# Kernel optimization log

Hardware: AMD Instinct MI355X
Metric: run time of the kernel (lower is better)

Reference implementation:

```python
import jax, jax.numpy as jnp
import numpy as np

B, F, V, DW, H, K, T = 32, 2048, 12000, 300, 512, 3, 32
START_ID, END_ID = 1, 2
NEG = -1e9


def lstm(x, h, c, Wx, Wh, b):
    # BasicLSTMCell with forget_bias=1.0
    z = x @ Wx + h @ Wh + b  # [N, 4H]
    i, f, g, o = jnp.split(z, 4, axis=-1)
    c2 = jax.nn.sigmoid(f + 1.0) * c + jax.nn.sigmoid(i) * jnp.tanh(g)
    h2 = jax.nn.sigmoid(o) * jnp.tanh(c2)
    return h2, c2


def beam_decode(E, Wx, Wh, b, Wl, bl, img):
    Bn = img.shape[0]
    img_t = jnp.repeat(img, K, axis=0)  # tile_batch: [B*K, F]
    h = jnp.zeros((Bn * K, H), img.dtype)
    c = jnp.zeros_like(h)
    beam_lp = jnp.tile(jnp.array([0.0] + [NEG] * (K - 1), img.dtype), (Bn, 1))  # [B,K]
    prev = jnp.full((Bn, K), START_ID, jnp.int32)
    finished = jnp.zeros((Bn, K), bool)
    lengths = jnp.zeros((Bn, K), jnp.int32)
    ids = jnp.zeros((Bn, K, T), jnp.int32)
    end_row = jnp.where(jnp.arange(V) == END_ID, 0.0, NEG)  # finished beams only emit END

    def step(carry, t):
        h, c, beam_lp, prev, finished, lengths, ids = carry
        x = jnp.concatenate([E[prev.reshape(-1)], img_t], axis=-1)  # [B*K, DW+F]
        h2, c2 = lstm(x, h, c, Wx, Wh, b)
        lp = jax.nn.log_softmax(h2 @ Wl + bl).reshape(Bn, K, V)
        lp = jnp.where(finished[:, :, None], end_row, lp)
        total = (beam_lp[:, :, None] + lp).reshape(Bn, K * V)
        scores, idx = jax.lax.top_k(total, K)  # [B,K]
        parent = idx // V
        word = (idx % V).astype(jnp.int32)
        g2 = lambda a: jnp.take_along_axis(a, parent, axis=1)
        g3 = lambda a: jnp.take_along_axis(a, parent[:, :, None], axis=1)
        h2 = g3(h2.reshape(Bn, K, H)).reshape(Bn * K, H)
        c2 = g3(c2.reshape(Bn, K, H)).reshape(Bn * K, H)
        ids = g3(ids).at[:, :, t].set(word)  # reorder hypotheses, append word
        fin_p = g2(finished)
        len_p = g2(lengths)
        lengths = jnp.where(fin_p, len_p, len_p + 1)
        finished = fin_p | (word == END_ID)
        return (h2, c2, scores, word, finished, lengths, ids), None

    carry, _ = jax.lax.scan(step, (h, c, beam_lp, prev, finished, lengths, ids), jnp.arange(T))
    return carry[6], carry[5]  # ids [B,K,T], lengths [B,K]


def teacher_rnn(E, Wx, Wh, b, img_t, seq_inputs, lengths):
    # dynamic_rnn semantics: zero outputs and frozen state past sequence_length
    N, L = seq_inputs.shape
    emb = E[seq_inputs]  # [N, L, DW]
    h0 = jnp.zeros((N, H), E.dtype)
    c0 = jnp.zeros_like(h0)

    def step(carry, xs):
        h, c = carry
        x_t, t = xs
        xin = jnp.concatenate([x_t, img_t], axis=-1)
        h2, c2 = lstm(xin, h, c, Wx, Wh, b)
        active = (t < lengths)[:, None]
        h = jnp.where(active, h2, h)
        c = jnp.where(active, c2, c)
        return (h, c), jnp.where(active, h2, 0.0)

    _, outs = jax.lax.scan(step, (h0, c0), (emb.transpose(1, 0, 2), jnp.arange(L)))
    return outs.transpose(1, 0, 2)  # [N, L, H]


def setup_inputs() -> dict:
    key = jax.random.key(0)
    ks = jax.random.split(key, 6)
    return {
        "mean_image_features": jax.random.normal(ks[0], (B, F), jnp.float32),
        "embeddings": jax.random.normal(ks[1], (V, DW), jnp.float32) * 0.1,
        "Wx": jax.random.normal(ks[2], (DW + F, 4 * H), jnp.float32) / np.sqrt(DW + F),
        "Wh": jax.random.normal(ks[3], (H, 4 * H), jnp.float32) / np.sqrt(H),
        "b_lstm": jnp.zeros((4 * H,), jnp.float32),
        "W_logits": jax.random.normal(ks[4], (H, V), jnp.float32) / np.sqrt(H),
        "b_logits": jnp.zeros((V,), jnp.float32),
    }


def reference(mean_image_features, embeddings, Wx, Wh, b_lstm, W_logits, b_logits):
    Bn = mean_image_features.shape[0]
    ids, lengths = beam_decode(embeddings, Wx, Wh, b_lstm, W_logits, b_logits, mean_image_features)
    seq_inputs = jnp.concatenate(
        [jnp.full((Bn, K, 1), START_ID, jnp.int32), ids], axis=2
    ).reshape(Bn * K, T + 1)
    img_t = jnp.repeat(mean_image_features, K, axis=0)
    acts = teacher_rnn(embeddings, Wx, Wh, b_lstm, img_t, seq_inputs, lengths.reshape(-1))
    logits = (acts @ W_logits + b_logits).reshape(Bn, K, T + 1, V)
    return logits, jnp.argmax(logits, axis=-1).astype(jnp.int32)
```

## Files before the change

kernel.cpp:

```cpp
#include <hip/hip_runtime.h>
#include <hip/hip_bf16.h>
#include <math.h>

#define NB   32
#define FDIM 2048
#define VV   12000
#define DWW  300
#define HH   512
#define KW   3
#define TDEC 32
#define SEQ  33
#define NK   96
#define G4   2048
#define START_ID 1
#define END_ID   2
#define NROWS 3168
#define NLB   188
#define INTMX 0x7fffffff
#define FLOORF (-3.0e38f)

typedef float f4v __attribute__((ext_vector_type(4)));
__device__ __forceinline__ void nt_store4(float* p, float4 v){
  f4v t; t.x=v.x; t.y=v.y; t.z=v.z; t.w=v.w;
  __builtin_nontemporal_store(t, (f4v*)p);
}

__device__ __forceinline__ float sigf(float x){ return 1.0f/(1.0f+expf(-x)); }

__device__ __forceinline__ unsigned short f2b(float x){
  __hip_bfloat16 b = __float2bfloat16(x);
  return *reinterpret_cast<unsigned short*>(&b);
}

__device__ __forceinline__ void ins3(float v, int i, float tv[3], int ti[3]){
  if (v > tv[0] || (v == tv[0] && i < ti[0])){
    tv[2]=tv[1]; ti[2]=ti[1]; tv[1]=tv[0]; ti[1]=ti[0]; tv[0]=v; ti[0]=i;
  } else if (v > tv[1] || (v == tv[1] && i < ti[1])){
    tv[2]=tv[1]; ti[2]=ti[1]; tv[1]=v; ti[1]=i;
  } else if (v > tv[2] || (v == tv[2] && i < ti[2])){
    tv[2]=v; ti[2]=i;
  }
}

__device__ __forceinline__ void flag_arrive(int* cnt){
  __hip_atomic_fetch_add(cnt, 1, __ATOMIC_RELEASE, __HIP_MEMORY_SCOPE_AGENT);
}
__device__ __forceinline__ void flag_wait(int* cnt, int target){
  while (__hip_atomic_load(cnt, __ATOMIC_ACQUIRE, __HIP_MEMORY_SCOPE_AGENT) < target)
    __builtin_amdgcn_s_sleep(1);
}

struct SArgs {
  const float *E, *Wx, *Wh, *Wl, *blog;
  float *P, *c2, *h2s, *zp, *partA, *beam_lp, *rowamax;
  int *prev, *finished, *lengths, *parst;
  int *cnt0, *cnt1;
  void *Lst;
};

__global__ __launch_bounds__(128) void k_pimg(const float* __restrict__ img,
                                              const float* __restrict__ Wx,
                                              float* __restrict__ parts)
{
  int colb = blockIdx.x, fb = blockIdx.y, tid = threadIdx.x;
  int col = colb*128 + tid;
  int f0 = fb*128;
  __shared__ float s_img[32][128];
  for (int r=0;r<32;r++) s_img[r][tid] = img[r*FDIM + f0 + tid];
  __syncthreads();
  float acc[32];
  #pragma unroll
  for (int r=0;r<32;r++) acc[r]=0.f;
  for (int f2=0; f2<128; ++f2){
    float w = Wx[(size_t)(DWW + f0 + f2)*G4 + col];
    #pragma unroll
    for (int r=0;r<32;r++) acc[r] += w * s_img[r][f2];
  }
  #pragma unroll
  for (int r=0;r<32;r++) parts[(size_t)fb*(32*G4) + r*G4 + col] = acc[r];
}

__global__ __launch_bounds__(512) void k_prep(const float* __restrict__ parts,
    const float* __restrict__ bls, const float* __restrict__ blog,
    float* __restrict__ P, float* __restrict__ beam_lp, int* __restrict__ prev,
    int* __restrict__ finished, int* __restrict__ lengths, int* __restrict__ cnts,
    float* __restrict__ bamax)
{
  int bid = blockIdx.x, tid = threadIdx.x;
  int gid = bid*512 + tid;
  float s = bls[gid & (G4-1)];
  for (int fb=0; fb<16; ++fb) s += parts[(size_t)fb*(32*G4) + gid];
  P[gid] = s;
  if (bid==0 && tid<NK){
    beam_lp[tid] = (tid%KW==0)?0.f:-1e9f;
    prev[tid]=START_ID; finished[tid]=0; lengths[tid]=0;
  }
  if (bid==1 && tid<2*TDEC) cnts[tid]=0;
  if (bid==2){
    __shared__ float s_rf[8]; __shared__ int s_ri[8];
    float bv=FLOORF; int bi=INTMX;
    for (int i=tid;i<VV;i+=512){
      float v=blog[i];
      if (v>bv || (v==bv && i<bi)){ bv=v; bi=i; }
    }
    #pragma unroll
    for (int d=1;d<64;d<<=1){
      float ov=__shfl_xor(bv,d); int oi=__shfl_xor(bi,d);
      if (ov>bv || (ov==bv && oi<bi)){ bv=ov; bi=oi; }
    }
    if ((tid&63)==0){ s_rf[tid>>6]=bv; s_ri[tid>>6]=bi; }
    __syncthreads();
    if (tid==0){
      for (int w=1;w<8;w++)
        if (s_rf[w]>bv || (s_rf[w]==bv && s_ri[w]<bi)){ bv=s_rf[w]; bi=s_ri[w]; }
      bamax[0] = (float)bi;
    }
  }
}

__global__ __launch_bounds__(512) void k_step1(SArgs a, int t)
{
  int bid = blockIdx.x, tid = threadIdx.x;
  __shared__ float smem[96*17 + 16*64];
  __shared__ int sprev[NK], spar[NK];
  if (t>0 && tid<NK){ sprev[tid]=a.prev[tid]; spar[tid]=a.parst[(t-1)*NK+tid]; }
  __syncthreads();

  {
    int colblk = bid & 31, p = bid >> 5;
    int col0 = colblk*64;
    int ks = p*104, ke = ks+104; if (ke>812) ke=812;
    float* sA = smem;
    float* sB = smem + 96*17;
    int tx = tid&15, ty = tid>>4;
    float4 acc[3];
    #pragma unroll
    for (int r=0;r<3;r++) acc[r]=make_float4(0.f,0.f,0.f,0.f);
    for (int k0=ks;k0<ke;k0+=16){
      int bk = ke-k0; if (bk>16) bk=16;
      for (int i=tid;i<96*16;i+=512){
        int n=i>>4, kk=i&15;
        float v=0.f;
        if (kk<bk){
          int kg=k0+kk;
          if (kg<DWW){
            int w = (t==0)?START_ID:sprev[n];
            v = a.E[(size_t)w*DWW+kg];
          } else if (t>0){
            v = a.h2s[((size_t)(t-1)*NK + spar[n])*HH + (kg-DWW)];
          }
        }
        sA[n*17+kk]=v;
      }
      for (int i=tid;i<16*64;i+=512){
        int kk=i>>6, cc=i&63;
        float v=0.f;
        if (kk<bk){
          int kg=k0+kk;
          v = (kg<DWW) ? a.Wx[(size_t)kg*G4+col0+cc] : a.Wh[(size_t)(kg-DWW)*G4+col0+cc];
        }
        sB[i]=v;
      }
      __syncthreads();
      #pragma unroll
      for (int kk=0;kk<16;++kk){
        float4 b4 = *(const float4*)&sB[kk*64+tx*4];
        #pragma unroll
        for (int rr=0;rr<3;rr++){
          float av = sA[(ty+rr*32)*17+kk];
          acc[rr].x += av*b4.x; acc[rr].y += av*b4.y;
          acc[rr].z += av*b4.z; acc[rr].w += av*b4.w;
        }
      }
      __syncthreads();
    }
    float* zpp = a.zp + (size_t)p*NK*G4;
    #pragma unroll
    for (int rr=0;rr<3;rr++)
      *(float4*)&zpp[(size_t)(ty+rr*32)*G4 + col0 + tx*4] = acc[rr];
  }
  __syncthreads();
  if (tid==0) flag_arrive(&a.cnt0[t]);
  if (bid >= NK) return;

  if (tid==0) flag_wait(&a.cnt0[t], 256);
  __syncthreads();
  {
    int n = bid, m = tid, bb = n/KW;
    const float* Pr = a.P + (size_t)bb*G4;
    float zi=Pr[m], zf=Pr[HH+m], zg=Pr[2*HH+m], zo=Pr[3*HH+m];
    for (int p=0;p<8;p++){
      const float* zz = a.zp + (size_t)p*NK*G4 + (size_t)n*G4;
      zi+=zz[m]; zf+=zz[HH+m]; zg+=zz[2*HH+m]; zo+=zz[3*HH+m];
    }
    float cold = (t==0) ? 0.f : a.c2[(size_t)((t-1)&1)*NK*HH + (size_t)spar[n]*HH + m];
    float c2v = sigf(zf+1.0f)*cold + sigf(zi)*tanhf(zg);
    float h2v = sigf(zo)*tanhf(c2v);
    a.c2[(size_t)(t&1)*NK*HH + (size_t)n*HH + m] = c2v;
    a.h2s[((size_t)t*NK+n)*HH + m] = h2v;
  }
}

template<int BF>
__global__ __launch_bounds__(512) void k_step2(SArgs a, int t)
{
  int bid = blockIdx.x, tid = threadIdx.x;
  __shared__ float smem[96*36 + 32*64];
  __shared__ float s_lse[KW], s_tv3[KW*3];
  __shared__ int   s_ti3[KW*3];

  {
    int col0 = bid*64;
    float* sA = smem;
    float* sB = smem + 96*36;
    int tx=tid&15, ty=tid>>4;
    float4 acc[3];
    #pragma unroll
    for (int r=0;r<3;r++) acc[r]=make_float4(0.f,0.f,0.f,0.f);
    for (int k0=0;k0<HH;k0+=32){
      for (int i=tid;i<768;i+=512){
        int row=i>>3, kq=(i&7)*4;
        *(float4*)&sA[row*36+kq] = *(const float4*)&a.h2s[((size_t)t*NK+row)*HH + k0+kq];
      }
      {
        int kk=tid>>4, c4=(tid&15)*4;
        int col=col0+c4;
        float4 v = make_float4(0.f,0.f,0.f,0.f);
        if (col < VV) v = *(const float4*)&a.Wl[(size_t)(k0+kk)*VV+col];
        *(float4*)&sB[kk*64+c4]=v;
      }
      __syncthreads();
      #pragma unroll
      for (int kk=0;kk<32;++kk){
        float4 b4 = *(const float4*)&sB[kk*64+tx*4];
        #pragma unroll
        for (int rr=0;rr<3;rr++){
          float av = sA[(ty+rr*32)*36+kk];
          acc[rr].x += av*b4.x; acc[rr].y += av*b4.y;
          acc[rr].z += av*b4.z; acc[rr].w += av*b4.w;
        }
      }
      __syncthreads();
    }
    int colg = col0 + tx*4;
    bool cval = colg < VV;
    float4 bias = make_float4(0.f,0.f,0.f,0.f);
    if (cval) bias = *(const float4*)&a.blog[colg];
    #pragma unroll
    for (int rr=0;rr<3;rr++){
      int row = ty + rr*32;
      float v0,v1,v2,v3;
      if (cval){
        v0=acc[rr].x+bias.x; v1=acc[rr].y+bias.y;
        v2=acc[rr].z+bias.z; v3=acc[rr].w+bias.w;
        size_t off = (size_t)(t*NK+row)*VV + colg;
        if (BF){
          ushort4 u;
          u.x=f2b(v0); u.y=f2b(v1); u.z=f2b(v2); u.w=f2b(v3);
          *(ushort4*)((unsigned short*)a.Lst + off) = u;
        } else {
          *(float4*)((float*)a.Lst + off) = make_float4(v0,v1,v2,v3);
        }
      } else { v0=v1=v2=v3=-INFINITY; }
      float m = fmaxf(fmaxf(v0,v1),fmaxf(v2,v3));
      #pragma unroll
      for (int d=1;d<16;d<<=1) m = fmaxf(m,__shfl_xor(m,d));
      float tv[3]={-INFINITY,-INFINITY,-INFINITY};
      int   ti[3]={INTMX,INTMX,INTMX};
      float s=0.f;
      if (cval){
        ins3(v0,colg,tv,ti); ins3(v1,colg+1,tv,ti);
        ins3(v2,colg+2,tv,ti); ins3(v3,colg+3,tv,ti);
        s = expf(v0-m)+expf(v1-m)+expf(v2-m)+expf(v3-m);
      }
      #pragma unroll
      for (int d=1;d<16;d<<=1){
        s += __shfl_xor(s,d);
        float p0=__shfl_xor(tv[0],d),p1=__shfl_xor(tv[1],d),p2=__shfl_xor(tv[2],d);
        int q0=__shfl_xor(ti[0],d),q1=__shfl_xor(ti[1],d),q2=__shfl_xor(ti[2],d);
        ins3(p0,q0,tv,ti); ins3(p1,q1,tv,ti); ins3(p2,q2,tv,ti);
      }
      if (tx==0){
        float* rp = a.partA + ((size_t)row*NLB + bid)*8;
        *(float4*)rp = make_float4(m,s,tv[0],tv[1]);
        *((float4*)rp+1) = make_float4(tv[2],__int_as_float(ti[0]),__int_as_float(ti[1]),__int_as_float(ti[2]));
      }
    }
  }
  __syncthreads();
  if (tid==0) flag_arrive(&a.cnt1[t]);
  if (bid >= NB) return;

  if (tid==0) flag_wait(&a.cnt1[t], NLB);
  __syncthreads();
  {
    int b = bid;
    int wv = tid>>6, lane = tid&63;
    if (wv < KW){
      int n = b*KW+wv;
      float M=FLOORF, S=0.f;
      float tv[3]={FLOORF,FLOORF,FLOORF}; int ti[3]={INTMX,INTMX,INTMX};
      for (int i=lane;i<NLB;i+=64){
        const float* rp = a.partA + ((size_t)n*NLB+i)*8;
        float4 r0=*(const float4*)rp, r1=*((const float4*)rp+1);
        float nm = fmaxf(M,r0.x);
        S = S*expf(M-nm) + r0.y*expf(r0.x-nm);
        M = nm;
        ins3(r0.z,__float_as_int(r1.y),tv,ti);
        ins3(r0.w,__float_as_int(r1.z),tv,ti);
        ins3(r1.x,__float_as_int(r1.w),tv,ti);
      }
      #pragma unroll
      for (int d=1;d<64;d<<=1){
        float Mo=__shfl_xor(M,d), So=__shfl_xor(S,d);
        float nm=fmaxf(M,Mo);
        S = S*expf(M-nm)+So*expf(Mo-nm);
        M=nm;
        float p0=__shfl_xor(tv[0],d),p1=__shfl_xor(tv[1],d),p2=__shfl_xor(tv[2],d);
        int q0=__shfl_xor(ti[0],d),q1=__shfl_xor(ti[1],d),q2=__shfl_xor(ti[2],d);
        ins3(p0,q0,tv,ti); ins3(p1,q1,tv,ti); ins3(p2,q2,tv,ti);
      }
      if (lane==0){
        s_lse[wv] = M + logf(S);
        #pragma unroll
        for (int j=0;j<3;j++){ s_tv3[wv*3+j]=tv[j]; s_ti3[wv*3+j]=ti[j]; }
        a.rowamax[t*NK+n] = (float)ti[0];
      }
    }
    __syncthreads();
    if (tid==0){
      float cv[3]={FLOORF,FLOORF,FLOORF}; int cf[3]={INTMX,INTMX,INTMX};
      for (int k=0;k<KW;k++){
        int n=b*KW+k;
        if (a.finished[n]){
          ins3(a.beam_lp[n], k*VV+END_ID, cv,cf);
        } else {
          float blp=a.beam_lp[n], lse=s_lse[k];
          for (int j=0;j<3;j++)
            ins3(blp + (s_tv3[k*3+j]-lse), k*VV+s_ti3[k*3+j], cv,cf);
        }
      }
      int fin_old[KW], len_old[KW];
      for (int j=0;j<KW;j++){ fin_old[j]=a.finished[b*KW+j]; len_old[j]=a.lengths[b*KW+j]; }
      for (int kp=0;kp<KW;kp++){
        int par=cf[kp]/VV, word=cf[kp]-par*VV;
        a.beam_lp[b*KW+kp]=cv[kp];
        a.prev[b*KW+kp]=word;
        a.parst[t*NK + b*KW+kp] = b*KW+par;
        int fp=fin_old[par];
        a.lengths[b*KW+kp] = fp?len_old[par]:(len_old[par]+1);
        a.finished[b*KW+kp] = fp | (word==END_ID);
      }
    }
  }
}

__global__ __launch_bounds__(128) void k_backtrack(const int* __restrict__ parst,
                                                   const int* __restrict__ lengths,
                                                   int* __restrict__ rowsrc)
{
  int n = threadIdx.x;
  if (n >= NK) return;
  int b = n / KW;
  int len = lengths[n];
  rowsrc[n*SEQ + TDEC] = -1;
  int a = n;
  for (int tau = TDEC-1; tau >= 1; --tau){
    int p = parst[tau*NK + a];
    rowsrc[n*SEQ + tau] = (tau < len) ? (tau*NK + p) : -1;
    a = p;
  }
  rowsrc[n*SEQ + 0] = b*KW;
}

template<int BF>
__global__ __launch_bounds__(512) void k_gather(const void* __restrict__ Lst,
    const int* __restrict__ rowsrc, const float* __restrict__ rowamax,
    const float* __restrict__ bamax, const float* __restrict__ blog,
    float* __restrict__ out)
{
  int row = blockIdx.x, tid = threadIdx.x;
  int src = rowsrc[row];
  float* orow = out + (size_t)row*VV;
  if (src >= 0){
    if (BF){
      const unsigned short* L = (const unsigned short*)Lst + (size_t)src*VV;
      for (int j=tid;j<VV/4;j+=512){
        ushort4 u = *(const ushort4*)&L[j*4];
        float4 v;
        v.x = __uint_as_float(((unsigned)u.x)<<16);
        v.y = __uint_as_float(((unsigned)u.y)<<16);
        v.z = __uint_as_float(((unsigned)u.z)<<16);
        v.w = __uint_as_float(((unsigned)u.w)<<16);
        nt_store4(&orow[j*4], v);
      }
    } else {
      const float* L = (const float*)Lst + (size_t)src*VV;
      for (int j=tid;j<VV/4;j+=512){
        float4 v = *(const float4*)&L[j*4];
        nt_store4(&orow[j*4], v);
      }
    }
    if (tid==0) out[(size_t)NROWS*VV + row] = rowamax[src];
  } else {
    for (int j=tid;j<VV/4;j+=512){
      float4 v = *(const float4*)&blog[j*4];
      nt_store4(&orow[j*4], v);
    }
    if (tid==0) out[(size_t)NROWS*VV + row] = bamax[0];
  }
}

extern "C" void kernel_launch(void* const* d_in, const int* in_sizes, int n_in,
                              void* d_out, int out_size, void* d_ws, size_t ws_size,
                              hipStream_t stream) {
  (void)in_sizes; (void)n_in; (void)out_size;
  const float* img  = (const float*)d_in[0];
  const float* E    = (const float*)d_in[1];
  const float* Wx   = (const float*)d_in[2];
  const float* Wh   = (const float*)d_in[3];
  const float* bls  = (const float*)d_in[4];
  const float* Wl   = (const float*)d_in[5];
  const float* blog = (const float*)d_in[6];
  float* out = (float*)d_out;

  float* ws = (float*)d_ws;
  size_t o = 0;
  float* P       = ws+o; o += (size_t)NB*G4;
  float* c2      = ws+o; o += (size_t)2*NK*HH;
  float* h2s     = ws+o; o += (size_t)TDEC*NK*HH;
  float* zp      = ws+o; o += (size_t)8*NK*G4;
  float* partA   = ws+o; o += (size_t)NK*NLB*8;
  float* beam_lp = ws+o; o += 128;
  float* rowamax = ws+o; o += (size_t)TDEC*NK;
  float* bamax   = ws+o; o += 4;
  int* prev      = (int*)(ws+o); o += 128;
  int* finished  = (int*)(ws+o); o += 128;
  int* lengths   = (int*)(ws+o); o += 128;
  int* parst     = (int*)(ws+o); o += (size_t)TDEC*NK;
  int* rowsrc    = (int*)(ws+o); o += 3328;
  int* cnts      = (int*)(ws+o); o += 64;
  o = (o+3) & ~(size_t)3;
  void* Lst      = (void*)(ws+o);

  bool f32 = (ws_size/4 > o) && ((ws_size/4 - o) >= (size_t)TDEC*NK*VV);

  SArgs a;
  a.E=E; a.Wx=Wx; a.Wh=Wh; a.Wl=Wl; a.blog=blog;
  a.P=P; a.c2=c2; a.h2s=h2s; a.zp=zp; a.partA=partA;
  a.beam_lp=beam_lp; a.rowamax=rowamax;
  a.prev=prev; a.finished=finished; a.lengths=lengths; a.parst=parst;
  a.cnt0=cnts; a.cnt1=cnts+TDEC;
  a.Lst=Lst;

  k_pimg<<<dim3(16,16),128,0,stream>>>(img, Wx, zp);
  k_prep<<<128,512,0,stream>>>(zp, bls, blog, P, beam_lp, prev, finished, lengths, cnts, bamax);

  if (f32){
    for (int t=0;t<TDEC;t++){
      k_step1<<<256,512,0,stream>>>(a,t);
      k_step2<0><<<NLB,512,0,stream>>>(a,t);
    }
    k_backtrack<<<1,128,0,stream>>>(parst, lengths, rowsrc);
    k_gather<0><<<NROWS,512,0,stream>>>(Lst,rowsrc,rowamax,bamax,blog,out);
  } else {
    for (int t=0;t<TDEC;t++){
      k_step1<<<256,512,0,stream>>>(a,t);
      k_step2<1><<<NLB,512,0,stream>>>(a,t);
    }
    k_backtrack<<<1,128,0,stream>>>(parst, lengths, rowsrc);
    k_gather<1><<<NROWS,512,0,stream>>>(Lst,rowsrc,rowamax,bamax,blog,out);
  }
}
```

Baseline: 3.069 ms.

## Split fused step kernels into separate launches instead of atomic-flag grid sync

Replaces the in-kernel atomic counter spin-waits, where the last blocks waited for all blocks to finish the GEMM, with four separate kernel launches per decode step (z GEMM, gate update, logits GEMM, beam select). It also switches the fp32 logits store to a nontemporal store. This removes spin-waiting and atomic traffic but doubles per-step launch count, adding launch overhead and kernel-boundary gaps across 32 steps.

```diff
diff --git a/kernel.cpp b/kernel.cpp
--- a/kernel.cpp
+++ b/kernel.cpp
@@ -42,19 +42,10 @@
   }
 }
 
-__device__ __forceinline__ void flag_arrive(int* cnt){
-  __hip_atomic_fetch_add(cnt, 1, __ATOMIC_RELEASE, __HIP_MEMORY_SCOPE_AGENT);
-}
-__device__ __forceinline__ void flag_wait(int* cnt, int target){
-  while (__hip_atomic_load(cnt, __ATOMIC_ACQUIRE, __HIP_MEMORY_SCOPE_AGENT) < target)
-    __builtin_amdgcn_s_sleep(1);
-}
-
 struct SArgs {
   const float *E, *Wx, *Wh, *Wl, *blog;
   float *P, *c2, *h2s, *zp, *partA, *beam_lp, *rowamax;
-  int *prev, *finished, *lengths, *parst;
-  int *cnt0, *cnt1;
+  int *prev, *finished, *lengths, *parst, *rowsrc;
   void *Lst;
 };
 
@@ -83,8 +74,7 @@
 __global__ __launch_bounds__(512) void k_prep(const float* __restrict__ parts,
     const float* __restrict__ bls, const float* __restrict__ blog,
     float* __restrict__ P, float* __restrict__ beam_lp, int* __restrict__ prev,
-    int* __restrict__ finished, int* __restrict__ lengths, int* __restrict__ cnts,
-    float* __restrict__ bamax)
+    int* __restrict__ finished, int* __restrict__ lengths, float* __restrict__ bamax)
 {
   int bid = blockIdx.x, tid = threadIdx.x;
   int gid = bid*512 + tid;
@@ -95,7 +85,6 @@
     beam_lp[tid] = (tid%KW==0)?0.f:-1e9f;
     prev[tid]=START_ID; finished[tid]=0; lengths[tid]=0;
   }
-  if (bid==1 && tid<2*TDEC) cnts[tid]=0;
   if (bid==2){
     __shared__ float s_rf[8]; __shared__ int s_ri[8];
     float bv=FLOORF; int bi=INTMX;
@@ -118,7 +107,7 @@
   }
 }
 
-__global__ __launch_bounds__(512) void k_step1(SArgs a, int t)
+__global__ __launch_bounds__(512) void k_z(SArgs a, int t)
 {
   int bid = blockIdx.x, tid = threadIdx.x;
   __shared__ float smem[96*17 + 16*64];
@@ -126,231 +115,220 @@
   if (t>0 && tid<NK){ sprev[tid]=a.prev[tid]; spar[tid]=a.parst[(t-1)*NK+tid]; }
   __syncthreads();
 
-  {
-    int colblk = bid & 31, p = bid >> 5;
-    int col0 = colblk*64;
-    int ks = p*104, ke = ks+104; if (ke>812) ke=812;
-    float* sA = smem;
-    float* sB = smem + 96*17;
-    int tx = tid&15, ty = tid>>4;
-    float4 acc[3];
-    #pragma unroll
-    for (int r=0;r<3;r++) acc[r]=make_float4(0.f,0.f,0.f,0.f);
-    for (int k0=ks;k0<ke;k0+=16){
-      int bk = ke-k0; if (bk>16) bk=16;
-      for (int i=tid;i<96*16;i+=512){
-        int n=i>>4, kk=i&15;
-        float v=0.f;
-        if (kk<bk){
-          int kg=k0+kk;
-          if (kg<DWW){
-            int w = (t==0)?START_ID:sprev[n];
-            v = a.E[(size_t)w*DWW+kg];
-          } else if (t>0){
-            v = a.h2s[((size_t)(t-1)*NK + spar[n])*HH + (kg-DWW)];
-          }
+  int colblk = bid & 31, p = bid >> 5;
+  int col0 = colblk*64;
+  int ks = p*104, ke = ks+104; if (ke>812) ke=812;
+  float* sA = smem;
+  float* sB = smem + 96*17;
+  int tx = tid&15, ty = tid>>4;
+  float4 acc[3];
+  #pragma unroll
+  for (int r=0;r<3;r++) acc[r]=make_float4(0.f,0.f,0.f,0.f);
+  for (int k0=ks;k0<ke;k0+=16){
+    int bk = ke-k0; if (bk>16) bk=16;
+    for (int i=tid;i<96*16;i+=512){
+      int n=i>>4, kk=i&15;
+      float v=0.f;
+      if (kk<bk){
+        int kg=k0+kk;
+        if (kg<DWW){
+          int w = (t==0)?START_ID:sprev[n];
+          v = a.E[(size_t)w*DWW+kg];
+        } else if (t>0){
+          v = a.h2s[((size_t)(t-1)*NK + spar[n])*HH + (kg-DWW)];
         }
-        sA[n*17+kk]=v;
-      }
-      for (int i=tid;i<16*64;i+=512){
-        int kk=i>>6, cc=i&63;
-        float v=0.f;
-        if (kk<bk){
-          int kg=k0+kk;
-          v = (kg<DWW) ? a.Wx[(size_t)kg*G4+col0+cc] : a.Wh[(size_t)(kg-DWW)*G4+col0+cc];
-        }
-        sB[i]=v;
-      }
-      __syncthreads();
+      }
+      sA[n*17+kk]=v;
+    }
+    for (int i=tid;i<16*64;i+=512){
+      int kk=i>>6, cc=i&63;
+      float v=0.f;
+      if (kk<bk){
+        int kg=k0+kk;
+        v = (kg<DWW) ? a.Wx[(size_t)kg*G4+col0+cc] : a.Wh[(size_t)(kg-DWW)*G4+col0+cc];
+      }
+      sB[i]=v;
+    }
+    __syncthreads();
+    #pragma unroll
+    for (int kk=0;kk<16;++kk){
+      float4 b4 = *(const float4*)&sB[kk*64+tx*4];
       #pragma unroll
-      for (int kk=0;kk<16;++kk){
-        float4 b4 = *(const float4*)&sB[kk*64+tx*4];
-        #pragma unroll
-        for (int rr=0;rr<3;rr++){
-          float av = sA[(ty+rr*32)*17+kk];
-          acc[rr].x += av*b4.x; acc[rr].y += av*b4.y;
-          acc[rr].z += av*b4.z; acc[rr].w += av*b4.w;
-        }
-      }
-      __syncthreads();
-    }
-    float* zpp = a.zp + (size_t)p*NK*G4;
-    #pragma unroll
-    for (int rr=0;rr<3;rr++)
-      *(float4*)&zpp[(size_t)(ty+rr*32)*G4 + col0 + tx*4] = acc[rr];
-  }
-  __syncthreads();
-  if (tid==0) flag_arrive(&a.cnt0[t]);
-  if (bid >= NK) return;
-
-  if (tid==0) flag_wait(&a.cnt0[t], 256);
-  __syncthreads();
-  {
-    int n = bid, m = tid, bb = n/KW;
-    const float* Pr = a.P + (size_t)bb*G4;
-    float zi=Pr[m], zf=Pr[HH+m], zg=Pr[2*HH+m], zo=Pr[3*HH+m];
-    for (int p=0;p<8;p++){
-      const float* zz = a.zp + (size_t)p*NK*G4 + (size_t)n*G4;
-      zi+=zz[m]; zf+=zz[HH+m]; zg+=zz[2*HH+m]; zo+=zz[3*HH+m];
-    }
-    float cold = (t==0) ? 0.f : a.c2[(size_t)((t-1)&1)*NK*HH + (size_t)spar[n]*HH + m];
-    float c2v = sigf(zf+1.0f)*cold + sigf(zi)*tanhf(zg);
-    float h2v = sigf(zo)*tanhf(c2v);
-    a.c2[(size_t)(t&1)*NK*HH + (size_t)n*HH + m] = c2v;
-    a.h2s[((size_t)t*NK+n)*HH + m] = h2v;
-  }
+      for (int rr=0;rr<3;rr++){
+        float av = sA[(ty+rr*32)*17+kk];
+        acc[rr].x += av*b4.x; acc[rr].y += av*b4.y;
+        acc[rr].z += av*b4.z; acc[rr].w += av*b4.w;
+      }
+    }
+    __syncthreads();
+  }
+  float* zpp = a.zp + (size_t)p*NK*G4;
+  #pragma unroll
+  for (int rr=0;rr<3;rr++)
+    *(float4*)&zpp[(size_t)(ty+rr*32)*G4 + col0 + tx*4] = acc[rr];
+}
+
+__global__ __launch_bounds__(512) void k_g(SArgs a, int t)
+{
+  int n = blockIdx.x, m = threadIdx.x;
+  int bb = n/KW;
+  int par = (t>0) ? a.parst[(t-1)*NK + n] : 0;
+  const float* Pr = a.P + (size_t)bb*G4;
+  float zi=Pr[m], zf=Pr[HH+m], zg=Pr[2*HH+m], zo=Pr[3*HH+m];
+  for (int p=0;p<8;p++){
+    const float* zz = a.zp + (size_t)p*NK*G4 + (size_t)n*G4;
+    zi+=zz[m]; zf+=zz[HH+m]; zg+=zz[2*HH+m]; zo+=zz[3*HH+m];
+  }
+  float cold = (t==0) ? 0.f : a.c2[(size_t)((t-1)&1)*NK*HH + (size_t)par*HH + m];
+  float c2v = sigf(zf+1.0f)*cold + sigf(zi)*tanhf(zg);
+  float h2v = sigf(zo)*tanhf(c2v);
+  a.c2[(size_t)(t&1)*NK*HH + (size_t)n*HH + m] = c2v;
+  a.h2s[((size_t)t*NK+n)*HH + m] = h2v;
 }
 
 template<int BF>
-__global__ __launch_bounds__(512) void k_step2(SArgs a, int t)
-{
-  int bid = blockIdx.x, tid = threadIdx.x;
+__global__ __launch_bounds__(512) void k_l(SArgs a, int t)
+{
   __shared__ float smem[96*36 + 32*64];
+  const int bid = blockIdx.x, tid = threadIdx.x;
+  const int col0 = bid*64;
+  float* sAl = smem;
+  float* sBl = smem + 96*36;
+  const int tx=tid&15, ty=tid>>4;
+  float4 acc[3];
+  #pragma unroll
+  for (int r=0;r<3;r++) acc[r]=make_float4(0.f,0.f,0.f,0.f);
+  for (int k0=0;k0<HH;k0+=32){
+    for (int i=tid;i<768;i+=512){
+      int row=i>>3, kq=(i&7)*4;
+      *(float4*)&sAl[row*36+kq] = *(const float4*)&a.h2s[((size_t)t*NK+row)*HH + k0+kq];
+    }
+    {
+      int kk=tid>>4, c4=(tid&15)*4;
+      int col=col0+c4;
+      float4 v = make_float4(0.f,0.f,0.f,0.f);
+      if (col < VV) v = *(const float4*)&a.Wl[(size_t)(k0+kk)*VV+col];
+      *(float4*)&sBl[kk*64+c4]=v;
+    }
+    __syncthreads();
+    #pragma unroll
+    for (int kk=0;kk<32;++kk){
+      float4 b4 = *(const float4*)&sBl[kk*64+tx*4];
+      #pragma unroll
+      for (int rr=0;rr<3;rr++){
+        float av = sAl[(ty+rr*32)*36+kk];
+        acc[rr].x += av*b4.x; acc[rr].y += av*b4.y;
+        acc[rr].z += av*b4.z; acc[rr].w += av*b4.w;
+      }
+    }
+    __syncthreads();
+  }
+  int colg = col0 + tx*4;
+  bool cval = colg < VV;
+  float4 bias = make_float4(0.f,0.f,0.f,0.f);
+  if (cval) bias = *(const float4*)&a.blog[colg];
+  #pragma unroll
+  for (int rr=0;rr<3;rr++){
+    int row = ty + rr*32;
+    float v0,v1,v2,v3;
+    if (cval){
+      v0=acc[rr].x+bias.x; v1=acc[rr].y+bias.y;
+      v2=acc[rr].z+bias.z; v3=acc[rr].w+bias.w;
+      size_t off = (size_t)(t*NK+row)*VV + colg;
+      if (BF){
+        ushort4 u;
+        u.x=f2b(v0); u.y=f2b(v1); u.z=f2b(v2); u.w=f2b(v3);
+        *(ushort4*)((unsigned short*)a.Lst + off) = u;
+      } else {
+        nt_store4((float*)a.Lst + off, make_float4(v0,v1,v2,v3));
+      }
+    } else { v0=v1=v2=v3=-INFINITY; }
+    float m = fmaxf(fmaxf(v0,v1),fmaxf(v2,v3));
+    #pragma unroll
+    for (int d=1;d<16;d<<=1) m = fmaxf(m,__shfl_xor(m,d));
+    float tv[3]={-INFINITY,-INFINITY,-INFINITY};
+    int   ti[3]={INTMX,INTMX,INTMX};
+    float s=0.f;
+    if (cval){
+      ins3(v0,colg,tv,ti); ins3(v1,colg+1,tv,ti);
+      ins3(v2,colg+2,tv,ti); ins3(v3,colg+3,tv,ti);
+      s = expf(v0-m)+expf(v1-m)+expf(v2-m)+expf(v3-m);
+    }
+    #pragma unroll
+    for (int d=1;d<16;d<<=1){
+      s += __shfl_xor(s,d);
+      float p0=__shfl_xor(tv[0],d),p1=__shfl_xor(tv[1],d),p2=__shfl_xor(tv[2],d);
+      int q0=__shfl_xor(ti[0],d),q1=__shfl_xor(ti[1],d),q2=__shfl_xor(ti[2],d);
+      ins3(p0,q0,tv,ti); ins3(p1,q1,tv,ti); ins3(p2,q2,tv,ti);
+    }
+    if (tx==0){
+      float* rp = a.partA + ((size_t)row*NLB + bid)*8;
+      *(float4*)rp = make_float4(m,s,tv[0],tv[1]);
+      *((float4*)rp+1) = make_float4(tv[2],__int_as_float(ti[0]),__int_as_float(ti[1]),__int_as_float(ti[2]));
+    }
+  }
+}
+
+__global__ __launch_bounds__(512) void k_s(SArgs a, int t)
+{
   __shared__ float s_lse[KW], s_tv3[KW*3];
   __shared__ int   s_ti3[KW*3];
-
-  {
-    int col0 = bid*64;
-    float* sA = smem;
-    float* sB = smem + 96*36;
-    int tx=tid&15, ty=tid>>4;
-    float4 acc[3];
-    #pragma unroll
-    for (int r=0;r<3;r++) acc[r]=make_float4(0.f,0.f,0.f,0.f);
-    for (int k0=0;k0<HH;k0+=32){
-      for (int i=tid;i<768;i+=512){
-        int row=i>>3, kq=(i&7)*4;
-        *(float4*)&sA[row*36+kq] = *(const float4*)&a.h2s[((size_t)t*NK+row)*HH + k0+kq];
-      }
-      {
-        int kk=tid>>4, c4=(tid&15)*4;
-        int col=col0+c4;
-        float4 v = make_float4(0.f,0.f,0.f,0.f);
-        if (col < VV) v = *(const float4*)&a.Wl[(size_t)(k0+kk)*VV+col];
-        *(float4*)&sB[kk*64+c4]=v;
-      }
-      __syncthreads();
+  int b = blockIdx.x, tid = threadIdx.x;
+  int wv = tid>>6, lane = tid&63;
+  if (wv < KW){
+    int n = b*KW+wv;
+    float M=FLOORF, S=0.f;
+    float tv[3]={FLOORF,FLOORF,FLOORF}; int ti[3]={INTMX,INTMX,INTMX};
+    for (int i=lane;i<NLB;i+=64){
+      const float* rp = a.partA + ((size_t)n*NLB+i)*8;
+      float4 r0=*(const float4*)rp, r1=*((const float4*)rp+1);
+      float nm = fmaxf(M,r0.x);
+      S = S*expf(M-nm) + r0.y*expf(r0.x-nm);
+      M = nm;
+      ins3(r0.z,__float_as_int(r1.y),tv,ti);
+      ins3(r0.w,__float_as_int(r1.z),tv,ti);
+      ins3(r1.x,__float_as_int(r1.w),tv,ti);
+    }
+    #pragma unroll
+    for (int d=1;d<64;d<<=1){
+      float Mo=__shfl_xor(M,d), So=__shfl_xor(S,d);
+      float nm=fmaxf(M,Mo);
+      S = S*expf(M-nm)+So*expf(Mo-nm);
+      M=nm;
+      float p0=__shfl_xor(tv[0],d),p1=__shfl_xor(tv[1],d),p2=__shfl_xor(tv[2],d);
+      int q0=__shfl_xor(ti[0],d),q1=__shfl_xor(ti[1],d),q2=__shfl_xor(ti[2],d);
+      ins3(p0,q0,tv,ti); ins3(p1,q1,tv,ti); ins3(p2,q2,tv,ti);
+    }
+    if (lane==0){
+      s_lse[wv] = M + logf(S);
       #pragma unroll
-      for (int kk=0;kk<32;++kk){
-        float4 b4 = *(const float4*)&sB[kk*64+tx*4];
-        #pragma unroll
-        for (int rr=0;rr<3;rr++){
-          float av = sA[(ty+rr*32)*36+kk];
-          acc[rr].x += av*b4.x; acc[rr].y += av*b4.y;
-          acc[rr].z += av*b4.z; acc[rr].w += av*b4.w;
-        }
-      }
-      __syncthreads();
-    }
-    int colg = col0 + tx*4;
-    bool cval = colg < VV;
-    float4 bias = make_float4(0.f,0.f,0.f,0.f);
-    if (cval) bias = *(const float4*)&a.blog[colg];
-    #pragma unroll
-    for (int rr=0;rr<3;rr++){
-      int row = ty + rr*32;
-      float v0,v1,v2,v3;
-      if (cval){
-        v0=acc[rr].x+bias.x; v1=acc[rr].y+bias.y;
-        v2=acc[rr].z+bias.z; v3=acc[rr].w+bias.w;
-        size_t off = (size_t)(t*NK+row)*VV + colg;
-        if (BF){
-          ushort4 u;
-          u.x=f2b(v0); u.y=f2b(v1); u.z=f2b(v2); u.w=f2b(v3);
-          *(ushort4*)((unsigned short*)a.Lst + off) = u;
-        } else {
-          *(float4*)((float*)a.Lst + off) = make_float4(v0,v1,v2,v3);
-        }
-      } else { v0=v1=v2=v3=-INFINITY; }
-      float m = fmaxf(fmaxf(v0,v1),fmaxf(v2,v3));
-      #pragma unroll
-      for (int d=1;d<16;d<<=1) m = fmaxf(m,__shfl_xor(m,d));
-      float tv[3]={-INFINITY,-INFINITY,-INFINITY};
-      int   ti[3]={INTMX,INTMX,INTMX};
-      float s=0.f;
-      if (cval){
-        ins3(v0,colg,tv,ti); ins3(v1,colg+1,tv,ti);
-        ins3(v2,colg+2,tv,ti); ins3(v3,colg+3,tv,ti);
-        s = expf(v0-m)+expf(v1-m)+expf(v2-m)+expf(v3-m);
-      }
-      #pragma unroll
-      for (int d=1;d<16;d<<=1){
-        s += __shfl_xor(s,d);
-        float p0=__shfl_xor(tv[0],d),p1=__shfl_xor(tv[1],d),p2=__shfl_xor(tv[2],d);
-        int q0=__shfl_xor(ti[0],d),q1=__shfl_xor(ti[1],d),q2=__shfl_xor(ti[2],d);
-        ins3(p0,q0,tv,ti); ins3(p1,q1,tv,ti); ins3(p2,q2,tv,ti);
-      }
-      if (tx==0){
-        float* rp = a.partA + ((size_t)row*NLB + bid)*8;
-        *(float4*)rp = make_float4(m,s,tv[0],tv[1]);
-        *((float4*)rp+1) = make_float4(tv[2],__int_as_float(ti[0]),__int_as_float(ti[1]),__int_as_float(ti[2]));
-      }
+      for (int j=0;j<3;j++){ s_tv3[wv*3+j]=tv[j]; s_ti3[wv*3+j]=ti[j]; }
+      a.rowamax[t*NK+n] = (float)ti[0];
     }
   }
   __syncthreads();
-  if (tid==0) flag_arrive(&a.cnt1[t]);
-  if (bid >= NB) return;
-
-  if (tid==0) flag_wait(&a.cnt1[t], NLB);
-  __syncthreads();
-  {
-    int b = bid;
-    int wv = tid>>6, lane = tid&63;
-    if (wv < KW){
-      int n = b*KW+wv;
-      float M=FLOORF, S=0.f;
-      float tv[3]={FLOORF,FLOORF,FLOORF}; int ti[3]={INTMX,INTMX,INTMX};
-      for (int i=lane;i<NLB;i+=64){
-        const float* rp = a.partA + ((size_t)n*NLB+i)*8;
-        float4 r0=*(const float4*)rp, r1=*((const float4*)rp+1);
-        float nm = fmaxf(M,r0.x);
-        S = S*expf(M-nm) + r0.y*expf(r0.x-nm);
-        M = nm;
-        ins3(r0.z,__float_as_int(r1.y),tv,ti);
-        ins3(r0.w,__float_as_int(r1.z),tv,ti);
-        ins3(r1.x,__float_as_int(r1.w),tv,ti);
-      }
-      #pragma unroll
-      for (int d=1;d<64;d<<=1){
-        float Mo=__shfl_xor(M,d), So=__shfl_xor(S,d);
-        float nm=fmaxf(M,Mo);
-        S = S*expf(M-nm)+So*expf(Mo-nm);
-        M=nm;
-        float p0=__shfl_xor(tv[0],d),p1=__shfl_xor(tv[1],d),p2=__shfl_xor(tv[2],d);
-        int q0=__shfl_xor(ti[0],d),q1=__shfl_xor(ti[1],d),q2=__shfl_xor(ti[2],d);
-        ins3(p0,q0,tv,ti); ins3(p1,q1,tv,ti); ins3(p2,q2,tv,ti);
-      }
-      if (lane==0){
-        s_lse[wv] = M + logf(S);
-        #pragma unroll
-        for (int j=0;j<3;j++){ s_tv3[wv*3+j]=tv[j]; s_ti3[wv*3+j]=ti[j]; }
-        a.rowamax[t*NK+n] = (float)ti[0];
-      }
-    }
-    __syncthreads();
-    if (tid==0){
-      float cv[3]={FLOORF,FLOORF,FLOORF}; int cf[3]={INTMX,INTMX,INTMX};
-      for (int k=0;k<KW;k++){
-        int n=b*KW+k;
-        if (a.finished[n]){
-          ins3(a.beam_lp[n], k*VV+END_ID, cv,cf);
-        } else {
-          float blp=a.beam_lp[n], lse=s_lse[k];
-          for (int j=0;j<3;j++)
-            ins3(blp + (s_tv3[k*3+j]-lse), k*VV+s_ti3[k*3+j], cv,cf);
-        }
-      }
-      int fin_old[KW], len_old[KW];
-      for (int j=0;j<KW;j++){ fin_old[j]=a.finished[b*KW+j]; len_old[j]=a.lengths[b*KW+j]; }
-      for (int kp=0;kp<KW;kp++){
-        int par=cf[kp]/VV, word=cf[kp]-par*VV;
-        a.beam_lp[b*KW+kp]=cv[kp];
-        a.prev[b*KW+kp]=word;
-        a.parst[t*NK + b*KW+kp] = b*KW+par;
-        int fp=fin_old[par];
-        a.lengths[b*KW+kp] = fp?len_old[par]:(len_old[par]+1);
-        a.finished[b*KW+kp] = fp | (word==END_ID);
-      }
+  if (tid==0){
+    float cv[3]={FLOORF,FLOORF,FLOORF}; int cf[3]={INTMX,INTMX,INTMX};
+    for (int k=0;k<KW;k++){
+      int n=b*KW+k;
+      if (a.finished[n]){
+        ins3(a.beam_lp[n], k*VV+END_ID, cv,cf);
+      } else {
+        float blp=a.beam_lp[n], lse=s_lse[k];
+        for (int j=0;j<3;j++)
+          ins3(blp + (s_tv3[k*3+j]-lse), k*VV+s_ti3[k*3+j], cv,cf);
+      }
+    }
+    int fin_old[KW], len_old[KW];
+    for (int j=0;j<KW;j++){ fin_old[j]=a.finished[b*KW+j]; len_old[j]=a.lengths[b*KW+j]; }
+    for (int kp=0;kp<KW;kp++){
+      int par=cf[kp]/VV, word=cf[kp]-par*VV;
+      a.beam_lp[b*KW+kp]=cv[kp];
+      a.prev[b*KW+kp]=word;
+      a.parst[t*NK + b*KW+kp] = b*KW+par;
+      int fp=fin_old[par];
+      a.lengths[b*KW+kp] = fp?len_old[par]:(len_old[par]+1);
+      a.finished[b*KW+kp] = fp | (word==END_ID);
     }
   }
 }
@@ -439,7 +417,6 @@
   int* lengths   = (int*)(ws+o); o += 128;
   int* parst     = (int*)(ws+o); o += (size_t)TDEC*NK;
   int* rowsrc    = (int*)(ws+o); o += 3328;
-  int* cnts      = (int*)(ws+o); o += 64;
   o = (o+3) & ~(size_t)3;
   void* Lst      = (void*)(ws+o);
 
@@ -449,24 +426,27 @@
   a.E=E; a.Wx=Wx; a.Wh=Wh; a.Wl=Wl; a.blog=blog;
   a.P=P; a.c2=c2; a.h2s=h2s; a.zp=zp; a.partA=partA;
   a.beam_lp=beam_lp; a.rowamax=rowamax;
-  a.prev=prev; a.finished=finished; a.lengths=lengths; a.parst=parst;
-  a.cnt0=cnts; a.cnt1=cnts+TDEC;
+  a.prev=prev; a.finished=finished; a.lengths=lengths; a.parst=parst; a.rowsrc=rowsrc;
   a.Lst=Lst;
 
   k_pimg<<<dim3(16,16),128,0,stream>>>(img, Wx, zp);
-  k_prep<<<128,512,0,stream>>>(zp, bls, blog, P, beam_lp, prev, finished, lengths, cnts, bamax);
+  k_prep<<<128,512,0,stream>>>(zp, bls, blog, P, beam_lp, prev, finished, lengths, bamax);
 
   if (f32){
     for (int t=0;t<TDEC;t++){
-      k_step1<<<256,512,0,stream>>>(a,t);
-      k_step2<0><<<NLB,512,0,stream>>>(a,t);
+      k_z<<<256,512,0,stream>>>(a,t);
+      k_g<<<NK,512,0,stream>>>(a,t);
+      k_l<0><<<NLB,512,0,stream>>>(a,t);
+      k_s<<<NB,512,0,stream>>>(a,t);
     }
     k_backtrack<<<1,128,0,stream>>>(parst, lengths, rowsrc);
     k_gather<0><<<NROWS,512,0,stream>>>(Lst,rowsrc,rowamax,bamax,blog,out);
   } else {
     for (int t=0;t<TDEC;t++){
-      k_step1<<<256,512,0,stream>>>(a,t);
-      k_step2<1><<<NLB,512,0,stream>>>(a,t);
+      k_z<<<256,512,0,stream>>>(a,t);
+      k_g<<<NK,512,0,stream>>>(a,t);
+      k_l<1><<<NLB,512,0,stream>>>(a,t);
+      k_s<<<NB,512,0,stream>>>(a,t);
     }
     k_backtrack<<<1,128,0,stream>>>(parst, lengths, rowsrc);
     k_gather<1><<<NROWS,512,0,stream>>>(Lst,rowsrc,rowamax,bamax,blog,out);
```

After: 2.608 ms. 1.18x faster.
